# Kernel tuning notes

Measured on AMD Instinct MI355X. Metric: run time of the kernel, lower is better.

## Reference

```python
import jax, jax.numpy as jnp
import numpy as np
from jax import lax

B = 8            # IMAGES_PER_GPU
A = 261888       # num_anchors (1024x1024 Mask R-CNN FPN anchors)
PRE_NMS_LIMIT = 6000
PROPOSAL_COUNT = 1000
NMS_THRESHOLD = 0.7


def setup_inputs() -> dict:
    key = jax.random.key(0)
    k1, k2, k3, k4 = jax.random.split(key, 4)
    rpn_probs = jax.random.uniform(k1, (B, A, 2), dtype=jnp.float32)
    rpn_bbox = jax.random.normal(k2, (B, A, 4), dtype=jnp.float32)
    # valid normalized anchors: y1,x1 in [0,0.9], height/width in [0.01,0.1]
    yx = jax.random.uniform(k3, (B, A, 2), minval=0.0, maxval=0.9)
    hw = jax.random.uniform(k4, (B, A, 2), minval=0.01, maxval=0.1)
    anchors = jnp.concatenate([yx, yx + hw], axis=-1)  # (y1, x1, y2, x2)
    return {"rpn_probs": rpn_probs, "rpn_bbox": rpn_bbox, "anchors": anchors}


def _apply_box_deltas(boxes, deltas):
    # boxes, deltas: [..., 4] in (y1, x1, y2, x2) / (dy, dx, log(dh), log(dw))
    h = boxes[..., 2] - boxes[..., 0]
    w = boxes[..., 3] - boxes[..., 1]
    cy = boxes[..., 0] + 0.5 * h + deltas[..., 0] * h
    cx = boxes[..., 1] + 0.5 * w + deltas[..., 1] * w
    h = h * jnp.exp(deltas[..., 2])
    w = w * jnp.exp(deltas[..., 3])
    y1 = cy - 0.5 * h
    x1 = cx - 0.5 * w
    return jnp.stack([y1, x1, y1 + h, x1 + w], axis=-1)


def _nms_single(boxes, scores):
    # boxes: [K, 4] already sorted by score descending; greedy NMS, zero-padded
    areas = (boxes[:, 2] - boxes[:, 0]) * (boxes[:, 3] - boxes[:, 1])

    def step(valid, _):
        idx = jnp.argmax(valid)          # first still-valid = highest score
        has = valid[idx]                 # False when no candidates remain
        box = boxes[idx]
        yy1 = jnp.maximum(box[0], boxes[:, 0])
        xx1 = jnp.maximum(box[1], boxes[:, 1])
        yy2 = jnp.minimum(box[2], boxes[:, 2])
        xx2 = jnp.minimum(box[3], boxes[:, 3])
        inter = jnp.maximum(yy2 - yy1, 0.0) * jnp.maximum(xx2 - xx1, 0.0)
        union = (box[2] - box[0]) * (box[3] - box[1]) + areas - inter
        iou = lax.stop_gradient(jnp.where(union > 0, inter / union, 0.0))
        valid = valid & (iou <= NMS_THRESHOLD)  # also suppresses idx (self IoU = 1)
        return valid, jnp.where(has, box, jnp.zeros_like(box))

    _, selected = lax.scan(step, jnp.ones(boxes.shape[0], dtype=bool), None,
                           length=PROPOSAL_COUNT)
    return selected  # [PROPOSAL_COUNT, 4], zero-padded like tf.pad in original


def reference(rpn_probs, rpn_bbox, anchors):
    std = jnp.asarray([0.1, 0.1, 0.2, 0.2], dtype=rpn_bbox.dtype)  # RPN_BBOX_STD_DEV
    scores = rpn_probs[:, :, 1]                 # fg prob [B, A]
    deltas = rpn_bbox * std
    k = min(PRE_NMS_LIMIT, anchors.shape[1])
    top_scores, ix = lax.top_k(scores, k)       # sorted descending, [B, K]
    idx = ix[..., None]
    deltas_k = jnp.take_along_axis(deltas, idx, axis=1)    # [B, K, 4]
    anchors_k = jnp.take_along_axis(anchors, idx, axis=1)  # [B, K, 4]
    boxes = jnp.clip(_apply_box_deltas(anchors_k, deltas_k), 0.0, 1.0)  # window [0,0,1,1]
    return jax.vmap(_nms_single)(boxes, top_scores)  # [B, PROPOSAL_COUNT, 4]
```

## Files before the change

kernel.cpp:

```cpp
#include <hip/hip_runtime.h>
#include <math.h>
#include <stdint.h>

typedef uint32_t u32; typedef uint64_t u64; typedef uint16_t u16; typedef int32_t i32;

#define BATCH 8
#define NA    261888
#define SEGS  16
#define SEGCHUNK 16368
#define WCHUNK 4092
#define SUBCAP 128
#define TOPK  6000
#define PROP  1000
#define TOP1  1024
#define SORTN 2048
#define CACHEB 8192
#define FBMAX 16384
#define MW32  32
#define PSTATIC 0x3F7C0000u

#define OFF_FBK   0
#define OFF_CACHE 1048576
#define OFF_CNT   1572864
#define OFF_STAT  1574912
#define OFF_BOX   1575040
#define OFF_AREA  1706112
#define OFF_MASK  1738880
#define WS_NEEDED 2787456


__device__ __forceinline__ void decode_box(const float4 an, const float4 dl,
                                           float4& bx, float& ar) {
    float d0 = __fmul_rn(dl.x, 0.1f), d1 = __fmul_rn(dl.y, 0.1f);
    float d2 = __fmul_rn(dl.z, 0.2f), d3 = __fmul_rn(dl.w, 0.2f);
    float h = __fsub_rn(an.z, an.x), w = __fsub_rn(an.w, an.y);
    float cy = __fadd_rn(__fadd_rn(an.x, __fmul_rn(0.5f, h)), __fmul_rn(d0, h));
    float cx = __fadd_rn(__fadd_rn(an.y, __fmul_rn(0.5f, w)), __fmul_rn(d1, w));
    float h2 = __fmul_rn(h, (float)exp((double)d2));
    float w2 = __fmul_rn(w, (float)exp((double)d3));
    float y1 = __fsub_rn(cy, __fmul_rn(0.5f, h2));
    float x1 = __fsub_rn(cx, __fmul_rn(0.5f, w2));
    float y2 = __fadd_rn(y1, h2);
    float x2 = __fadd_rn(x1, w2);
    y1 = fminf(fmaxf(y1, 0.f), 1.f); x1 = fminf(fmaxf(x1, 0.f), 1.f);
    y2 = fminf(fmaxf(y2, 0.f), 1.f); x2 = fminf(fmaxf(x2, 0.f), 1.f);
    bx = make_float4(y1, x1, y2, x2);
    ar = __fmul_rn(__fsub_rn(y2, y1), __fsub_rn(x2, x1));
}

__device__ __forceinline__ bool sup_pred(const float4 bi, const float ai,
                                         const float4 bj, const float aj) {
    const double tmid = (double)0.7f + 0x1p-25;
    float yy1 = fmaxf(bi.x, bj.x), xx1 = fmaxf(bi.y, bj.y);
    float yy2 = fminf(bi.z, bj.z), xx2 = fminf(bi.w, bj.w);
    float ih = fmaxf(__fsub_rn(yy2, yy1), 0.f);
    float iw = fmaxf(__fsub_rn(xx2, xx1), 0.f);
    float inter = __fmul_rn(ih, iw);
    float uni = __fsub_rn(__fadd_rn(ai, aj), inter);
    return (uni > 0.f) && ((double)inter >= tmid * (double)uni);
}

__global__ __launch_bounds__(256) void k_histcache(const float4* __restrict__ p4,
                                                   u64* __restrict__ cache,
                                                   u32* __restrict__ cnt) {
    const int b = blockIdx.y, seg = blockIdx.x;
    const int wave = threadIdx.x >> 6, lane = threadIdx.x & 63;
    const u64 lmask = (1ull << lane) - 1ull;
    const size_t fbase = ((size_t)b * NA + seg * SEGCHUNK + wave * WCHUNK) >> 1;
    const u32 abase = (u32)(seg * SEGCHUNK + wave * WCHUNK);
    u64* cseg = cache + (size_t)b * CACHEB + (seg * 4 + wave) * SUBCAP;
    u32 wOff = 0;
    #pragma unroll 4
    for (int it = 0; it < 32; ++it) {
        int f = it * 64 + lane;
        bool ok = f < (WCHUNK / 2);
        u32 bitsA = 0, bitsB = 0;
        if (ok) {
            float4 v = p4[fbase + f];
            bitsA = __float_as_uint(v.y);
            bitsB = __float_as_uint(v.w);
        }
        bool pA = ok && bitsA >= PSTATIC;
        bool pB = ok && bitsB >= PSTATIC;
        u64 mA = __ballot(pA);
        u64 mB = __ballot(pB);
        u32 cA = (u32)__popcll(mA);
        if (pA) {
            u32 slot = wOff + (u32)__popcll(mA & lmask);
            if (slot < SUBCAP) cseg[slot] = ((u64)(~bitsA) << 32) | (u64)(abase + 2 * f);
        }
        if (pB) {
            u32 slot = wOff + cA + (u32)__popcll(mB & lmask);
            if (slot < SUBCAP) cseg[slot] = ((u64)(~bitsB) << 32) | (u64)(abase + 2 * f + 1);
        }
        wOff += cA + (u32)__popcll(mB);
    }
    if (lane == 0) cnt[b * 64 + seg * 4 + wave] = wOff;
}

__global__ __launch_bounds__(1024) void k_sortdec(const u64* __restrict__ cache,
                                                  const u32* __restrict__ cnt,
                                                  const float4* __restrict__ anchors,
                                                  const float4* __restrict__ bbox,
                                                  u32* __restrict__ stat_g,
                                                  float4* __restrict__ boxes,
                                                  float* __restrict__ areas) {
    __shared__ u32 hist[4096];
    __shared__ u32 ps[256];
    __shared__ u64 s[SORTN];
    __shared__ u32 scnt[64];
    __shared__ u32 sP, sm, stat;
    const int b = blockIdx.x;
    const int tid = threadIdx.x;
    if (tid == 0) { stat = 1u; sm = 0; }
    for (int i = tid; i < 4096; i += 1024) hist[i] = 0;
    for (int i = tid; i < SORTN; i += 1024) s[i] = ~0ull;
    __syncthreads();
    if (tid < 64) {
        u32 raw = cnt[b * 64 + tid];
        scnt[tid] = raw > SUBCAP ? SUBCAP : raw;
        if (raw > SUBCAP) stat = 0u;
    }
    __syncthreads();
    for (int t = tid; t < CACHEB; t += 1024) {
        int sub = t >> 7, off = t & (SUBCAP - 1);
        if (off < (int)scnt[sub]) {
            u32 bits = ~((u32)(cache[(size_t)b * CACHEB + t] >> 32));
            atomicAdd(&hist[(bits >> 6) & 0xFFFu], 1u);
        }
    }
    __syncthreads();
    if (tid < 256) {
        u32 su = 0;
        for (int k = 0; k < 16; ++k) su += hist[tid * 16 + k];
        ps[tid] = su;
    }
    __syncthreads();
    if (tid == 0) {
        u32 acc = 0; int seg = -1;
        for (int t = 255; t >= 0; --t) {
            if (acc + ps[t] >= TOP1) { seg = t; break; }
            acc += ps[t];
        }
        if (seg < 0) { stat = 0u; sP = PSTATIC; }
        else {
            int bin = seg * 16; u32 g = acc;
            for (int k = 15; k >= 0; --k) {
                u32 c = hist[seg * 16 + k];
                if (g + c >= TOP1) { bin = seg * 16 + k; break; }
                g += c;
            }
            sP = PSTATIC + ((u32)bin << 6);
        }
    }
    __syncthreads();
    const u64 thrKey = ((u64)(~sP) << 32) | 0xFFFFFFFFull;
    for (int t = tid; t < CACHEB; t += 1024) {
        int sub = t >> 7, off = t & (SUBCAP - 1);
        if (off < (int)scnt[sub]) {
            u64 key = cache[(size_t)b * CACHEB + t];
            if (key <= thrKey) {
                u32 slot = atomicAdd(&sm, 1u);
                if (slot < SORTN) s[slot] = key;
            }
        }
    }
    __syncthreads();
    if (tid == 0 && (sm < TOP1 || sm > SORTN)) stat = 0u;
    for (int k = 2; k <= SORTN; k <<= 1) {
        for (int j = k >> 1; j > 0; j >>= 1) {
            int p = tid;
            int i = ((p & ~(j - 1)) << 1) | (p & (j - 1));
            int l = i | j;
            u64 a = s[i], c = s[l];
            bool up = ((i & k) == 0);
            if ((a > c) == up) { s[i] = c; s[l] = a; }
            __syncthreads();
        }
    }
    u32 idx = (u32)s[tid];
    float4 bx; float ar;
    if (idx == 0xFFFFFFFFu) { bx = make_float4(-5.f, -5.f, -5.f, -5.f); ar = 0.f; }
    else decode_box(anchors[(size_t)b * NA + idx], bbox[(size_t)b * NA + idx], bx, ar);
    boxes[b * TOP1 + tid] = bx;
    areas[b * TOP1 + tid] = ar;
    if (tid == 0) stat_g[b] = stat;
}


__global__ __launch_bounds__(256) void k_mask(const float4* __restrict__ boxes,
                                              const float* __restrict__ areas,
                                              u32* __restrict__ mt_all) {
    const int b = blockIdx.y;
    const int wave = threadIdx.x >> 6, lane = threadIdx.x & 63;
    const int i = blockIdx.x * 4 + wave;
    u32* mt = mt_all + (size_t)b * MW32 * TOP1;
    float4 bi = boxes[b * TOP1 + i];
    float  ai = areas[b * TOP1 + i];
    #pragma unroll
    for (int c = 0; c < 16; ++c) {
        float4 bj = boxes[b * TOP1 + c * 64 + lane];
        float  aj = areas[b * TOP1 + c * 64 + lane];
        u64 word = __ballot(sup_pred(bi, ai, bj, aj));
        if (lane == 0) {
            mt[(2 * c) * TOP1 + i]     = (u32)word;
            mt[(2 * c + 1) * TOP1 + i] = (u32)(word >> 32);
        }
    }
}

__global__ __launch_bounds__(1024) void k_nmsfb(const u32* __restrict__ mt_all,
                                                const float4* __restrict__ boxes,
                                                const float2* __restrict__ p2,
                                                const float4* __restrict__ bbox,
                                                const float4* __restrict__ anchors,
                                                const u32* __restrict__ stat_g,
                                                u64* __restrict__ fbkeys,
                                                float4* __restrict__ out) {
    __shared__ u32 valid[MW32];
    __shared__ u32 wpre[MW32 + 1];
    __shared__ u32 chg;
    const int b = blockIdx.x;
    const int i = threadIdx.x;
    const int wv = i >> 6, lane = i & 63;
    const int wi = i >> 5;
    const u32* mt = mt_all + (size_t)b * MW32 * TOP1;
    u32 row[MW32];
    #pragma unroll
    for (int w = 0; w < MW32; ++w) row[w] = 0;
    for (int w = 0; w < wi; ++w) row[w] = mt[w * TOP1 + i];
    row[wi] = mt[wi * TOP1 + i] & ((1u << (i & 31)) - 1u);
    if (i < MW32) valid[i] = 0xFFFFFFFFu;
    bool conv = false;
    for (int it = 0; it < 48; ++it) {
        __syncthreads();
        if (i == 0) chg = 0;
        u32 sup = 0;
        #pragma unroll
        for (int w = 0; w < MW32; ++w) sup |= valid[w] & row[w];
        u64 nb = __ballot(sup == 0u);
        __syncthreads();
        if (lane == 0) {
            u32 lo = (u32)nb, hi = (u32)(nb >> 32);
            if (valid[2 * wv] != lo)     { valid[2 * wv] = lo;     atomicOr(&chg, 1u); }
            if (valid[2 * wv + 1] != hi) { valid[2 * wv + 1] = hi; atomicOr(&chg, 1u); }
        }
        __syncthreads();
        if (chg == 0u) { conv = true; break; }
    }
    __syncthreads();
    if (i == 0) {
        u32 r = 0;
        for (int w = 0; w < MW32; ++w) { wpre[w] = r; r += __popc(valid[w]); }
        wpre[MW32] = r;
    }
    __syncthreads();
    u32 V = wpre[MW32];
    if (conv && V >= PROP && stat_g[b] != 0u) {
        u32 vw = valid[wi];
        bool isv = ((vw >> (i & 31)) & 1u) != 0;
        u32 rank = wpre[wi] + __popc(vw & ((1u << (i & 31)) - 1u));
        if (isv && rank < PROP) out[b * PROP + rank] = boxes[b * TOP1 + i];
        return;
    }
    __shared__ float4 abox[PROP];
    __shared__ float  aar[PROP];
    __shared__ u32 fh[4096];
    __shared__ u32 fps[256];
    __shared__ u32 nsh, sP6;
    if (i == 0) nsh = 0;
    for (int z = i; z < 4096; z += 1024) fh[z] = 0;
    __syncthreads();
    for (int a = i; a < NA; a += 1024) {
        u32 bits = __float_as_uint(p2[(size_t)b * NA + a].y);
        atomicAdd(&fh[bits >> 18], 1u);
    }
    __syncthreads();
    if (i < 256) {
        u32 su = 0;
        for (int k = 0; k < 16; ++k) su += fh[i * 16 + k];
        fps[i] = su;
    }
    __syncthreads();
    if (i == 0) {
        u32 acc = 0; int seg = 0;
        for (int t = 255; t >= 0; --t) { if (acc + fps[t] >= TOPK) { seg = t; break; } acc += fps[t]; }
        int b6 = seg * 16; u32 g6 = acc;
        for (int k = 15; k >= 0; --k) {
            u32 c = fh[seg * 16 + k];
            if (g6 + c >= TOPK) { b6 = seg * 16 + k; break; }
            g6 += c;
        }
        sP6 = (u32)b6 << 18;
    }
    __syncthreads();
    u32 P6 = sP6;
    for (int a = i; a < NA; a += 1024) {
        u32 bits = __float_as_uint(p2[(size_t)b * NA + a].y);
        if (bits >= P6) {
            u32 p = atomicAdd(&nsh, 1u);
            if (p < FBMAX) fbkeys[(size_t)b * FBMAX + p] = ((u64)(~bits) << 32) | (u64)a;
        }
    }
    __syncthreads();
    u32 n = nsh; if (n > FBMAX) n = FBMAX;
    volatile u64* vk = (volatile u64*)(fbkeys + (size_t)b * FBMAX);
    for (int i2 = (int)n + i; i2 < FBMAX; i2 += 1024) vk[i2] = ~0ull;
    __syncthreads();
    for (int k = 2; k <= FBMAX; k <<= 1) {
        for (int j = k >> 1; j > 0; j >>= 1) {
            for (int p = i; p < FBMAX / 2; p += 1024) {
                int ii = ((p & ~(j - 1)) << 1) | (p & (j - 1));
                int l = ii | j;
                u64 a = vk[ii], c = vk[l];
                bool up = ((ii & k) == 0);
                if ((a > c) == up) { vk[ii] = c; vk[l] = a; }
            }
            __syncthreads();
        }
    }
    int acc_n = 0;
    int limit = (int)n < TOPK ? (int)n : TOPK;
    for (int t = 0; t < limit && acc_n < PROP; ++t) {
        u32 idx = (u32)vk[t];
        float4 bi2; float ai2;
        decode_box(anchors[(size_t)b * NA + idx], bbox[(size_t)b * NA + idx], bi2, ai2);
        int pred = 0;
        if (i < acc_n) pred = sup_pred(bi2, ai2, abox[i], aar[i]) ? 1 : 0;
        int any = __syncthreads_or(pred);
        if (!any) {
            if (i == 0) {
                abox[acc_n] = bi2; aar[acc_n] = ai2;
                out[b * PROP + acc_n] = bi2;
            }
            ++acc_n;
            __syncthreads();
        }
    }
    for (int t = acc_n + i; t < PROP; t += 1024)
        out[b * PROP + t] = make_float4(0.f, 0.f, 0.f, 0.f);
}


extern "C" void kernel_launch(void* const* d_in, const int* in_sizes, int n_in,
                              void* d_out, int out_size, void* d_ws, size_t ws_size,
                              hipStream_t stream) {
    (void)in_sizes; (void)n_in; (void)out_size;
    if (ws_size < (size_t)WS_NEEDED) return;
    const float2* p2      = (const float2*)d_in[0];
    const float4* p4      = (const float4*)d_in[0];
    const float4* bbox    = (const float4*)d_in[1];
    const float4* anchors = (const float4*)d_in[2];
    float4* out = (float4*)d_out;

    char* ws = (char*)d_ws;
    u64* fbkeys  = (u64*)(ws + OFF_FBK);
    u64* cache   = (u64*)(ws + OFF_CACHE);
    u32* cnt     = (u32*)(ws + OFF_CNT);
    u32* stat_g  = (u32*)(ws + OFF_STAT);
    float4* boxes= (float4*)(ws + OFF_BOX);
    float* areas = (float*)(ws + OFF_AREA);
    u32* maskT   = (u32*)(ws + OFF_MASK);

    dim3 ghc(SEGS, BATCH), gmask(TOP1 / 4, BATCH);
    k_histcache<<<ghc,   256, 0, stream>>>(p4, cache, cnt);
    k_sortdec  <<<BATCH, 1024, 0, stream>>>(cache, cnt, anchors, bbox, stat_g, boxes, areas);
    k_mask     <<<gmask, 256, 0, stream>>>(boxes, areas, maskT);
    k_nmsfb    <<<BATCH, 1024, 0, stream>>>(maskT, boxes, p2, bbox, anchors, stat_g, fbkeys, out);
}
```

Before: 163.3 us.

## Replace bitonic sort with histogram bucket scatter and rank-by-count selection

The top-1024 selection in k_sortdec no longer runs a 2048-element bitonic sort with many barriers. It builds parallel suffix sums over the score histogram, finds the threshold bin in parallel, and scatters the keys into per-bin buckets. Each key then computes its final rank by counting smaller keys within its own bin. The NMS fixed-point loop also drops one barrier per iteration by using __syncthreads_or instead of a shared change flag. The cost of the rank step grows with bin occupancy, and the fallback path is taken if more than 2048 keys survive the threshold.

```diff
diff --git a/kernel.cpp b/kernel.cpp
--- a/kernel.cpp
+++ b/kernel.cpp
@@ -13,7 +13,7 @@
 #define TOPK  6000
 #define PROP  1000
 #define TOP1  1024
-#define SORTN 2048
+#define TMPCAP 2048
 #define CACHEB 8192
 #define FBMAX 16384
 #define MW32  32
@@ -106,15 +106,18 @@
                                                   float4* __restrict__ boxes,
                                                   float* __restrict__ areas) {
     __shared__ u32 hist[4096];
+    __shared__ u32 suffix[4096];
     __shared__ u32 ps[256];
-    __shared__ u64 s[SORTN];
+    __shared__ u32 psS[257];
+    __shared__ u64 tmp[TMPCAP];
     __shared__ u32 scnt[64];
-    __shared__ u32 sP, sm, stat;
+    __shared__ u32 wq[4];
+    __shared__ u32 sP, sN, sBin, stat;
     const int b = blockIdx.x;
     const int tid = threadIdx.x;
-    if (tid == 0) { stat = 1u; sm = 0; }
+    const int lane = tid & 63, wv = tid >> 6;
+    if (tid == 0) { stat = 1u; sBin = 0xFFFFFFFFu; }
     for (int i = tid; i < 4096; i += 1024) hist[i] = 0;
-    for (int i = tid; i < SORTN; i += 1024) s[i] = ~0ull;
     __syncthreads();
     if (tid < 64) {
         u32 raw = cnt[b * 64 + tid];
@@ -132,58 +135,90 @@
     __syncthreads();
     if (tid < 256) {
         u32 su = 0;
+        #pragma unroll
         for (int k = 0; k < 16; ++k) su += hist[tid * 16 + k];
         ps[tid] = su;
     }
     __syncthreads();
+    {
+        u32 v = (tid < 256) ? ps[tid] : 0u;
+        #pragma unroll
+        for (int d = 1; d < 64; d <<= 1) {
+            u32 o = __shfl_down(v, d);
+            if (lane + d < 64) v += o;
+        }
+        if (tid < 256 && lane == 0) wq[wv] = v;
+        __syncthreads();
+        if (tid < 256) {
+            u32 add = 0;
+            for (int q = wv + 1; q < 4; ++q) add += wq[q];
+            psS[tid] = v + add;
+        }
+        if (tid == 0) psS[256] = 0u;
+        __syncthreads();
+    }
+    {
+        const int t4 = tid * 4;
+        const int seg = tid >> 2;
+        const int segEnd = seg * 16 + 15;
+        u32 tail = 0;
+        for (int bb = t4 + 4; bb <= segEnd; ++bb) tail += hist[bb];
+        u32 h0 = hist[t4], h1 = hist[t4 + 1], h2 = hist[t4 + 2], h3 = hist[t4 + 3];
+        u32 s3 = psS[seg + 1] + tail;
+        u32 s2 = s3 + h3;
+        u32 s1 = s2 + h2;
+        u32 s0 = s1 + h1;
+        suffix[t4] = s0; suffix[t4 + 1] = s1; suffix[t4 + 2] = s2; suffix[t4 + 3] = s3;
+        if (s0 < TOP1 && s0 + h0 >= TOP1) sBin = (u32)t4;
+        if (s1 < TOP1 && s1 + h1 >= TOP1) sBin = (u32)(t4 + 1);
+        if (s2 < TOP1 && s2 + h2 >= TOP1) sBin = (u32)(t4 + 2);
+        if (s3 < TOP1 && s3 + h3 >= TOP1) sBin = (u32)(t4 + 3);
+    }
+    __syncthreads();
     if (tid == 0) {
-        u32 acc = 0; int seg = -1;
-        for (int t = 255; t >= 0; --t) {
-            if (acc + ps[t] >= TOP1) { seg = t; break; }
-            acc += ps[t];
-        }
-        if (seg < 0) { stat = 0u; sP = PSTATIC; }
+        if (sBin == 0xFFFFFFFFu) stat = 0u;
         else {
-            int bin = seg * 16; u32 g = acc;
-            for (int k = 15; k >= 0; --k) {
-                u32 c = hist[seg * 16 + k];
-                if (g + c >= TOP1) { bin = seg * 16 + k; break; }
-                g += c;
+            sP = PSTATIC + (sBin << 6);
+            u32 n = suffix[sBin] + hist[sBin];
+            sN = n;
+            if (n > TMPCAP) stat = 0u;
+        }
+    }
+    __syncthreads();
+    if (stat) {
+        for (int i = tid; i < 4096; i += 1024) hist[i] = 0;
+        __syncthreads();
+        const u32 P = sP;
+        for (int t = tid; t < CACHEB; t += 1024) {
+            int sub = t >> 7, off = t & (SUBCAP - 1);
+            if (off < (int)scnt[sub]) {
+                u64 key = cache[(size_t)b * CACHEB + t];
+                u32 bits = ~((u32)(key >> 32));
+                if (bits >= P) {
+                    u32 bin = (bits >> 6) & 0xFFFu;
+                    u32 arr = atomicAdd(&hist[bin], 1u);
+                    tmp[suffix[bin] + arr] = key;
+                }
             }
-            sP = PSTATIC + ((u32)bin << 6);
-        }
-    }
-    __syncthreads();
-    const u64 thrKey = ((u64)(~sP) << 32) | 0xFFFFFFFFull;
-    for (int t = tid; t < CACHEB; t += 1024) {
-        int sub = t >> 7, off = t & (SUBCAP - 1);
-        if (off < (int)scnt[sub]) {
-            u64 key = cache[(size_t)b * CACHEB + t];
-            if (key <= thrKey) {
-                u32 slot = atomicAdd(&sm, 1u);
-                if (slot < SORTN) s[slot] = key;
+        }
+        __syncthreads();
+        const u32 n = sN;
+        for (u32 t = (u32)tid; t < n; t += 1024) {
+            u64 key = tmp[t];
+            u32 bits = ~((u32)(key >> 32));
+            u32 bin = (bits >> 6) & 0xFFFu;
+            u32 base = suffix[bin], len = hist[bin];
+            u32 pos = base;
+            for (u32 q = base; q < base + len; ++q) pos += (tmp[q] < key) ? 1u : 0u;
+            if (pos < TOP1) {
+                u32 idx = (u32)key;
+                float4 bx; float ar;
+                decode_box(anchors[(size_t)b * NA + idx], bbox[(size_t)b * NA + idx], bx, ar);
+                boxes[b * TOP1 + pos] = bx;
+                areas[b * TOP1 + pos] = ar;
             }
         }
     }
-    __syncthreads();
-    if (tid == 0 && (sm < TOP1 || sm > SORTN)) stat = 0u;
-    for (int k = 2; k <= SORTN; k <<= 1) {
-        for (int j = k >> 1; j > 0; j >>= 1) {
-            int p = tid;
-            int i = ((p & ~(j - 1)) << 1) | (p & (j - 1));
-            int l = i | j;
-            u64 a = s[i], c = s[l];
-            bool up = ((i & k) == 0);
-            if ((a > c) == up) { s[i] = c; s[l] = a; }
-            __syncthreads();
-        }
-    }
-    u32 idx = (u32)s[tid];
-    float4 bx; float ar;
-    if (idx == 0xFFFFFFFFu) { bx = make_float4(-5.f, -5.f, -5.f, -5.f); ar = 0.f; }
-    else decode_box(anchors[(size_t)b * NA + idx], bbox[(size_t)b * NA + idx], bx, ar);
-    boxes[b * TOP1 + tid] = bx;
-    areas[b * TOP1 + tid] = ar;
     if (tid == 0) stat_g[b] = stat;
 }
 
@@ -219,7 +254,6 @@
                                                 float4* __restrict__ out) {
     __shared__ u32 valid[MW32];
     __shared__ u32 wpre[MW32 + 1];
-    __shared__ u32 chg;
     const int b = blockIdx.x;
     const int i = threadIdx.x;
     const int wv = i >> 6, lane = i & 63;
@@ -231,22 +265,19 @@
     for (int w = 0; w < wi; ++w) row[w] = mt[w * TOP1 + i];
     row[wi] = mt[wi * TOP1 + i] & ((1u << (i & 31)) - 1u);
     if (i < MW32) valid[i] = 0xFFFFFFFFu;
+    __syncthreads();
     bool conv = false;
     for (int it = 0; it < 48; ++it) {
-        __syncthreads();
-        if (i == 0) chg = 0;
         u32 sup = 0;
         #pragma unroll
         for (int w = 0; w < MW32; ++w) sup |= valid[w] & row[w];
         u64 nb = __ballot(sup == 0u);
+        u32 lo = (u32)nb, hi = (u32)(nb >> 32);
+        int changed = 0;
+        if (lane == 0) changed = (valid[2 * wv] != lo) | (valid[2 * wv + 1] != hi);
         __syncthreads();
-        if (lane == 0) {
-            u32 lo = (u32)nb, hi = (u32)(nb >> 32);
-            if (valid[2 * wv] != lo)     { valid[2 * wv] = lo;     atomicOr(&chg, 1u); }
-            if (valid[2 * wv + 1] != hi) { valid[2 * wv + 1] = hi; atomicOr(&chg, 1u); }
-        }
-        __syncthreads();
-        if (chg == 0u) { conv = true; break; }
+        if (lane == 0) { valid[2 * wv] = lo; valid[2 * wv + 1] = hi; }
+        if (!__syncthreads_or(changed)) { conv = true; break; }
     }
     __syncthreads();
     if (i == 0) {
```

New measurement: 152.5 us. 6.6% less time.
